# Kernel tuning notes

Measured on AMD Instinct MI355X. Metric: run time of the kernel, lower is better.

## Reference

```python
import jax, jax.numpy as jnp
import numpy as np

NUM_CLASSES = 4
NUM_PROTOTYPE = 8
D = 512
N = 200704  # 16 * 112 * 112 flattened tokens
GAMMA = 0.999        # EMA momentum (self.gamma)
EPS_SINK = 0.05      # sinkhorn epsilon
SINK_ITERS = 3       # sinkhorn iterations


def l2_normalize(x, axis=-1, eps=1e-12):
    n = jnp.linalg.norm(x, axis=axis, keepdims=True)
    return x / jnp.maximum(n, eps)


def layer_norm(x, g, b, eps=1e-5):
    mu = jnp.mean(x, axis=-1, keepdims=True)
    var = jnp.var(x, axis=-1, keepdims=True)
    return (x - mu) / jnp.sqrt(var + eps) * g + b


def masked_sinkhorn(scores, sel):
    # scores: [N, M] similarity to this class's prototypes; sel: [N] bool row mask
    # Faithful masked re-expression of distributed_sinkhorn (which gathers rows
    # where gt_seg == k); zeroed rows contribute nothing to any normalization.
    M = scores.shape[1]
    self32 = sel.astype(scores.dtype)[:, None]
    L = jnp.exp(scores / EPS_SINK) * self32           # [N, M]
    B = jnp.maximum(sel.sum(), 1).astype(scores.dtype)  # number of selected rows
    L = L / jnp.maximum(L.sum(), 1e-30)

    def body(L, _):
        col = L.sum(axis=0, keepdims=True)            # per-prototype mass
        L = L / jnp.maximum(col, 1e-30) / M
        row = L.sum(axis=1, keepdims=True)            # per-token mass
        L = (L / jnp.maximum(row, 1e-30) / B) * self32
        return L, None

    L, _ = jax.lax.scan(body, L, None, length=SINK_ITERS)
    L = L * B
    idx = jnp.argmax(L, axis=1)
    # hard one-hot assignment (deterministic stand-in for hard gumbel_softmax)
    q = jax.nn.one_hot(idx, M, dtype=scores.dtype) * self32
    return q


def prototype_learning(_c, pred, gt_seg, masks, protos, momentum):
    # _c [N, D], pred/gt_seg [N], masks [N, M, K], protos [K, M, D]
    correct = gt_seg == pred
    new_rows = []
    for k in range(NUM_CLASSES):  # small fixed class loop, as in the original
        sel = gt_seg == k
        q = masked_sinkhorn(masks[:, :, k], sel)      # [N, M]
        m_k = (correct & sel).astype(_c.dtype)        # [N]
        m_q = q * m_k[:, None]                        # masked assignments
        c_q = _c * m_k[:, None]                       # masked features
        f = m_q.T @ c_q                               # [M, D] aggregation
        n = m_q.sum(axis=0)                           # [M] per-prototype counts
        f = l2_normalize(f)
        upd = momentum * protos[k] + (1.0 - momentum) * f
        valid = (n != 0) & (sel.sum() > 0) & (n.sum() > 0)
        new_rows.append(jnp.where(valid[:, None], upd, protos[k]))
    return l2_normalize(jnp.stack(new_rows, axis=0))


def reference(feats, ln_gamma, ln_beta, mask_gamma, mask_beta, prototypes, gt_seg):
    _c = l2_normalize(layer_norm(feats, ln_gamma, ln_beta))       # [N, D]
    protos = l2_normalize(prototypes)                             # [K, M, D]
    masks = jnp.einsum('nd,kmd->nmk', _c, protos)                 # [N, M, K]
    out_seg = layer_norm(jnp.max(masks, axis=1), mask_gamma, mask_beta)  # [N, K]
    pred = jnp.argmax(out_seg, axis=1)
    new_protos = prototype_learning(_c, pred, gt_seg.astype(jnp.int32), masks, protos, GAMMA)
    return out_seg, new_protos


def setup_inputs() -> dict:
    key = jax.random.key(0)
    k1, k2, k3 = jax.random.split(key, 3)
    return {
        'feats': jax.random.normal(k1, (N, D), dtype=jnp.float32),
        'ln_gamma': jnp.ones((D,), jnp.float32),
        'ln_beta': jnp.zeros((D,), jnp.float32),
        'mask_gamma': jnp.ones((NUM_CLASSES,), jnp.float32),
        'mask_beta': jnp.zeros((NUM_CLASSES,), jnp.float32),
        'prototypes': 0.02 * jax.random.normal(k2, (NUM_CLASSES, NUM_PROTOTYPE, D), dtype=jnp.float32),
        'gt_seg': jax.random.randint(k3, (N,), 0, NUM_CLASSES, dtype=jnp.int32),
    }
```

## Files before the change

### kernel.cpp

```cpp
#include <hip/hip_runtime.h>
#include <hip/hip_bf16.h>
#include <math.h>

#define NROWS 200704
#define DIM 512
#define NKM 32

#define OFF_RED0   0
#define OFF_RED1   32
#define OFF_RED2   64
#define OFF_CNT    96
#define OFF_NP     100
#define OFF_CUR    192
#define OFF_BASE   2240
#define OFF_FACC   2304
#define ZERO_FLOATS 18688
#define OFF_SUMGP  18688
#define OFF_BP     18720
#define OFF_SCAL   18752
#define OFF_G2GB   18816
#define OFF_PROTON 19840
#define OFF_WHI    36224
#define OFF_WLO    44544
#define OFF_RSTATS 52864
#define OFF_E      855680
#define OFF_FLAGS  2461312
#define OFF_SORT   2662016

typedef __attribute__((ext_vector_type(8)))  short short8;
typedef __attribute__((ext_vector_type(16))) float f32x16;

union ABFrag { unsigned int u[4]; short8 s; };

__device__ __forceinline__ unsigned int pk2(float a, float b) {
    __hip_bfloat162 h2 = __float22bfloat162_rn(make_float2(a, b));
    union { __hip_bfloat162 h; unsigned int u; } cv;
    cv.h = h2;
    return cv.u;
}

__device__ __forceinline__ float block_reduce_sum(float v, float* sm) {
    int t = threadIdx.x;
    sm[t] = v; __syncthreads();
    #pragma unroll
    for (int o = 128; o > 0; o >>= 1) {
        if (t < o) sm[t] += sm[t + o];
        __syncthreads();
    }
    float r = sm[0]; __syncthreads();
    return r;
}

__global__ __launch_bounds__(256) void k_prep(const float* __restrict__ protos,
                                              const float* __restrict__ g,
                                              const float* __restrict__ b,
                                              float* __restrict__ ws) {
    __shared__ float sm[256];
    int t = threadIdx.x, j = blockIdx.x;
    if (j < NKM) {
        const float* p = protos + j * DIM;
        float v = p[t] * p[t] + p[t + 256] * p[t + 256];
        float ss = block_reduce_sum(v, sm);
        float den = fmaxf(sqrtf(ss), 1e-12f);
        float sgp = 0.f, sbp = 0.f;
        unsigned short* whi = (unsigned short*)ws + 2 * OFF_WHI + j * 520;
        unsigned short* wlo = (unsigned short*)ws + 2 * OFF_WLO + j * 520;
        for (int d = t; d < DIM; d += 256) {
            float pn = p[d] / den;
            ws[OFF_PROTON + j * DIM + d] = pn;
            float w = g[d] * pn;
            unsigned int hb = pk2(w, 0.f) & 0xffffu;
            float hf = __uint_as_float(hb << 16);
            unsigned int lb = pk2(w - hf, 0.f) & 0xffffu;
            whi[d] = (unsigned short)hb;
            wlo[d] = (unsigned short)lb;
            sgp += w; sbp += b[d] * pn;
        }
        float s1 = block_reduce_sum(sgp, sm);
        float s2 = block_reduce_sum(sbp, sm);
        if (t == 0) { ws[OFF_SUMGP + j] = s1; ws[OFF_BP + j] = s2; }
    } else {
        float a = 0.f, c = 0.f, e = 0.f;
        for (int d = t; d < DIM; d += 256) {
            float gv = g[d], bv = b[d];
            ws[OFF_G2GB + 2 * d]     = gv * gv;
            ws[OFF_G2GB + 2 * d + 1] = gv * bv;
            a += gv * gv; c += gv * bv; e += bv * bv;
        }
        float s1 = block_reduce_sum(a, sm);
        float s2 = block_reduce_sum(c, sm);
        float s3 = block_reduce_sum(e, sm);
        if (t == 0) { ws[OFF_SCAL] = s1; ws[OFF_SCAL + 1] = s2; ws[OFF_SCAL + 2] = s3; }
    }
}

#define ST1(XV, G2V, GBV) { float _x = (XV); float _x2 = _x * _x; \
    sx += _x; sxx += _x2; \
    sxg2  = fmaf(_x,  (G2V), sxg2); \
    sx2g2 = fmaf(_x2, (G2V), sx2g2); \
    sxgb  = fmaf(_x,  (GBV), sxgb); }

#define PAIRSPLIT(A0, B0, HO, LO) { \
    unsigned int _h = pk2((A0), (B0)); HO = _h; \
    float _ha = __uint_as_float(_h << 16); \
    float _hb = __uint_as_float(_h & 0xffff0000u); \
    LO = pk2((A0) - _ha, (B0) - _hb); }

__global__ __launch_bounds__(256, 2) void k_main(const float* __restrict__ feats,
                                                 const float* __restrict__ mg,
                                                 const float* __restrict__ mb,
                                                 const int* __restrict__ gt_seg,
                                                 float* __restrict__ ws,
                                                 float* __restrict__ out) {
    __shared__ __align__(16) unsigned short ls_whi[32 * 520];
    __shared__ __align__(16) unsigned short ls_wlo[32 * 520];
    __shared__ __align__(16) float ls_g2gb[1024];
    int t = threadIdx.x;
    {
        const float4* sh = (const float4*)(ws + OFF_WHI);
        float4* dh = (float4*)ls_whi;
        for (int i = t; i < 2080; i += 256) dh[i] = sh[i];
        const float4* sl = (const float4*)(ws + OFF_WLO);
        float4* dl = (float4*)ls_wlo;
        for (int i = t; i < 2080; i += 256) dl[i] = sl[i];
        const float4* sg = (const float4*)(ws + OFF_G2GB);
        float4* dg = (float4*)ls_g2gb;
        dg[t] = sg[t];
    }
    __syncthreads();

    int wv = t >> 6, l = t & 63;
    int h = l >> 5, c32 = l & 31;
    int row0 = blockIdx.x * 128 + wv * 32;
    const float* xrow = feats + (size_t)(row0 + c32) * DIM + h * 8;
    const unsigned short* bhp = ls_whi + c32 * 520 + h * 8;
    const unsigned short* blp = ls_wlo + c32 * 520 + h * 8;
    const float4* g4 = ((const float4*)ls_g2gb) + h * 4;

    f32x16 acc;
    #pragma unroll
    for (int i = 0; i < 16; ++i) acc[i] = 0.f;
    float sx = 0.f, sxx = 0.f, sxg2 = 0.f, sx2g2 = 0.f, sxgb = 0.f;

    #pragma unroll 4
    for (int kc = 0; kc < 32; ++kc) {
        float4 xa = *(const float4*)(xrow + kc * 16);
        float4 xb = *(const float4*)(xrow + kc * 16 + 4);
        float4 ga  = g4[kc * 8 + 0];
        float4 gb_ = g4[kc * 8 + 1];
        float4 gc  = g4[kc * 8 + 2];
        float4 gd  = g4[kc * 8 + 3];
        ST1(xa.x, ga.x,  ga.y)  ST1(xa.y, ga.z,  ga.w)
        ST1(xa.z, gb_.x, gb_.y) ST1(xa.w, gb_.z, gb_.w)
        ST1(xb.x, gc.x,  gc.y)  ST1(xb.y, gc.z,  gc.w)
        ST1(xb.z, gd.x,  gd.y)  ST1(xb.w, gd.z,  gd.w)
        ABFrag ah, al;
        PAIRSPLIT(xa.x, xa.y, ah.u[0], al.u[0])
        PAIRSPLIT(xa.z, xa.w, ah.u[1], al.u[1])
        PAIRSPLIT(xb.x, xb.y, ah.u[2], al.u[2])
        PAIRSPLIT(xb.z, xb.w, ah.u[3], al.u[3])
        short8 bh = *(const short8*)(bhp + kc * 16);
        short8 bl = *(const short8*)(blp + kc * 16);
        acc = __builtin_amdgcn_mfma_f32_32x32x16_bf16(ah.s, bh, acc, 0, 0, 0);
        acc = __builtin_amdgcn_mfma_f32_32x32x16_bf16(ah.s, bl, acc, 0, 0, 0);
        acc = __builtin_amdgcn_mfma_f32_32x32x16_bf16(al.s, bh, acc, 0, 0, 0);
    }

    sx    += __shfl_xor(sx, 32, 64);
    sxx   += __shfl_xor(sxx, 32, 64);
    sxg2  += __shfl_xor(sxg2, 32, 64);
    sx2g2 += __shfl_xor(sx2g2, 32, 64);
    sxgb  += __shfl_xor(sxgb, 32, 64);

    float scal0 = ws[OFF_SCAL], scal1 = ws[OFF_SCAL + 1], scal2 = ws[OFF_SCAL + 2];
    float mu  = sx * (1.0f / DIM);
    float var = sxx * (1.0f / DIM) - mu * mu;
    float istd = 1.0f / sqrtf(var + 1e-5f);
    float l2v = istd * istd * (sx2g2 - 2.0f * mu * sxg2 + mu * mu * scal0)
              + 2.0f * istd * (sxgb - mu * scal1) + scal2;
    float L = sqrtf(fmaxf(l2v, 0.0f));
    float invL = 1.0f / fmaxf(L, 1e-12f);
    float aa = istd * invL;
    if (l < 32)
        *(float4*)(ws + OFF_RSTATS + (size_t)(row0 + l) * 4) = make_float4(mu, istd, invL, 0.f);

    float wsum = ws[OFF_SUMGP + c32], wbp = ws[OFF_BP + c32];
    float mg0 = mg[0], mg1 = mg[1], mg2 = mg[2], mg3 = mg[3];
    float mb0 = mb[0], mb1 = mb[1], mb2 = mb[2], mb3 = mb[3];
    int q = c32 >> 3;
    int li8 = c32 & 7;

    #pragma unroll
    for (int r = 0; r < 16; ++r) {
        int rowt = (r & 3) + 8 * (r >> 2) + 4 * h;
        int grow = row0 + rowt;
        float mu_r = __shfl(mu, rowt, 64);
        float aa_r = __shfl(aa, rowt, 64);
        float il_r = __shfl(invL, rowt, 64);
        float s = aa_r * (acc[r] - mu_r * wsum) + il_r * wbp;
        float m = s;
        m = fmaxf(m, __shfl_xor(m, 1, 64));
        m = fmaxf(m, __shfl_xor(m, 2, 64));
        m = fmaxf(m, __shfl_xor(m, 4, 64));
        float vA = m;
        float vB = __shfl_xor(vA, 8, 64);
        float vC = __shfl_xor(vA, 16, 64);
        float vD = __shfl_xor(vB, 16, 64);
        float o0 = (q == 0) ? vA : (q == 1) ? vB : (q == 2) ? vC : vD;
        float o1 = (q == 1) ? vA : (q == 0) ? vB : (q == 3) ? vC : vD;
        float o2 = (q == 2) ? vA : (q == 3) ? vB : (q == 0) ? vC : vD;
        float o3 = (q == 3) ? vA : (q == 2) ? vB : (q == 1) ? vC : vD;
        float mu4 = 0.25f * (o0 + o1 + o2 + o3);
        float e0 = o0 - mu4, e1 = o1 - mu4, e2 = o2 - mu4, e3 = o3 - mu4;
        float v4 = 0.25f * (e0 * e0 + e1 * e1 + e2 * e2 + e3 * e3);
        float is4 = 1.0f / sqrtf(v4 + 1e-5f);
        float f0 = e0 * is4 * mg0 + mb0;
        float f1 = e1 * is4 * mg1 + mb1;
        float f2 = e2 * is4 * mg2 + mb2;
        float f3 = e3 * is4 * mg3 + mb3;
        int pred = 0; float bo = f0;
        if (f1 > bo) { bo = f1; pred = 1; }
        if (f2 > bo) { bo = f2; pred = 2; }
        if (f3 > bo) { bo = f3; pred = 3; }
        int gtv = gt_seg[grow] & 3;
        if (c32 == 0) {
            *(float4*)(out + (size_t)grow * 4) = make_float4(f0, f1, f2, f3);
            ((int*)ws)[OFF_FLAGS + grow] = gtv | ((pred == gtv) ? 4 : 0);
        }
        if (q == gtv) {
            float ev = expf(s * 20.0f);
            ws[OFF_E + (size_t)grow * 8 + li8] = ev;
        }
    }
}

__global__ __launch_bounds__(256) void k_red0(const int* __restrict__ gt_seg,
                                              float* __restrict__ ws) {
    __shared__ float lred[NKM];
    __shared__ int lcnt[4];
    int t = threadIdx.x;
    if (t < NKM) lred[t] = 0.f;
    if (t < 4) lcnt[t] = 0;
    __syncthreads();
    int row = blockIdx.x * 256 + t;
    int gt = gt_seg[row] & 3;
    float4 ea = *(const float4*)(ws + OFF_E + (size_t)row * 8);
    float4 eb = *(const float4*)(ws + OFF_E + (size_t)row * 8 + 4);
    atomicAdd(&lred[gt * 8 + 0], ea.x); atomicAdd(&lred[gt * 8 + 1], ea.y);
    atomicAdd(&lred[gt * 8 + 2], ea.z); atomicAdd(&lred[gt * 8 + 3], ea.w);
    atomicAdd(&lred[gt * 8 + 4], eb.x); atomicAdd(&lred[gt * 8 + 5], eb.y);
    atomicAdd(&lred[gt * 8 + 6], eb.z); atomicAdd(&lred[gt * 8 + 7], eb.w);
    atomicAdd(&lcnt[gt], 1);
    __syncthreads();
    if (t < NKM) atomicAdd(&ws[OFF_RED0 + t], lred[t]);
    if (t < 4) atomicAdd(&((int*)ws)[OFF_CNT + t], lcnt[t]);
}

__global__ __launch_bounds__(256) void k_red1(const int* __restrict__ gt_seg,
                                              float* __restrict__ ws) {
    __shared__ float S0p[4], Bk[4], a1[NKM], lred[NKM];
    int t = threadIdx.x;
    if (t < 4) {
        float s = 0.f;
        #pragma unroll
        for (int m = 0; m < 8; ++m) s += ws[OFF_RED0 + t * 8 + m];
        S0p[t] = fmaxf(s, 1e-30f);
        Bk[t] = fmaxf((float)((const int*)ws)[OFF_CNT + t], 1.0f);
    }
    if (t < NKM) lred[t] = 0.f;
    __syncthreads();
    if (t < NKM) {
        float col = ws[OFF_RED0 + t] / S0p[t >> 3];
        a1[t] = 1.0f / (fmaxf(col, 1e-30f) * 8.0f);
    }
    __syncthreads();
    int row = blockIdx.x * 256 + t;
    int gt = gt_seg[row] & 3;
    float4 ea = *(const float4*)(ws + OFF_E + (size_t)row * 8);
    float4 eb = *(const float4*)(ws + OFF_E + (size_t)row * 8 + 4);
    float ev[8] = {ea.x, ea.y, ea.z, ea.w, eb.x, eb.y, eb.z, eb.w};
    float dotv = 0.f;
    #pragma unroll
    for (int m = 0; m < 8; ++m) dotv += ev[m] * a1[gt * 8 + m];
    float row1 = dotv / S0p[gt];
    float r1 = 1.0f / (fmaxf(row1, 1e-30f) * Bk[gt]);
    #pragma unroll
    for (int m = 0; m < 8; ++m) atomicAdd(&lred[gt * 8 + m], ev[m] * r1);
    __syncthreads();
    if (t < NKM) atomicAdd(&ws[OFF_RED1 + t], lred[t]);
}

__global__ __launch_bounds__(256) void k_red2(const int* __restrict__ gt_seg,
                                              float* __restrict__ ws) {
    __shared__ float S0p[4], Bk[4], a1[NKM], a2[NKM], lred[NKM];
    int t = threadIdx.x;
    if (t < 4) {
        float s = 0.f;
        #pragma unroll
        for (int m = 0; m < 8; ++m) s += ws[OFF_RED0 + t * 8 + m];
        S0p[t] = fmaxf(s, 1e-30f);
        Bk[t] = fmaxf((float)((const int*)ws)[OFF_CNT + t], 1.0f);
    }
    if (t < NKM) lred[t] = 0.f;
    __syncthreads();
    if (t < NKM) {
        float col = ws[OFF_RED0 + t] / S0p[t >> 3];
        a1[t] = 1.0f / (fmaxf(col, 1e-30f) * 8.0f);
    }
    __syncthreads();
    if (t < NKM) {
        float col2 = a1[t] * ws[OFF_RED1 + t] / S0p[t >> 3];
        a2[t] = 1.0f / (fmaxf(col2, 1e-30f) * 8.0f);
    }
    __syncthreads();
    int row = blockIdx.x * 256 + t;
    int gt = gt_seg[row] & 3;
    float4 ea = *(const float4*)(ws + OFF_E + (size_t)row * 8);
    float4 eb = *(const float4*)(ws + OFF_E + (size_t)row * 8 + 4);
    float ev[8] = {ea.x, ea.y, ea.z, ea.w, eb.x, eb.y, eb.z, eb.w};
    float dotv = 0.f;
    #pragma unroll
    for (int m = 0; m < 8; ++m) dotv += ev[m] * a1[gt * 8 + m];
    float row1 = dotv / S0p[gt];
    float r1 = 1.0f / (fmaxf(row1, 1e-30f) * Bk[gt]);
    float dot2 = 0.f;
    #pragma unroll
    for (int m = 0; m < 8; ++m) dot2 += ev[m] * a1[gt * 8 + m] * a2[gt * 8 + m];
    float row2 = dot2 / S0p[gt] * r1;
    float r2 = 1.0f / (fmaxf(row2, 1e-30f) * Bk[gt]);
    #pragma unroll
    for (int m = 0; m < 8; ++m) atomicAdd(&lred[gt * 8 + m], ev[m] * r1 * r2);
    __syncthreads();
    if (t < NKM) atomicAdd(&ws[OFF_RED2 + t], lred[t]);
}

__global__ __launch_bounds__(256) void k_assign(float* __restrict__ ws) {
    __shared__ float S0p[4], Bk[4], a1[NKM], a2[NKM], F[NKM];
    __shared__ int ln[NKM];
    int t = threadIdx.x;
    if (t < 4) {
        float s = 0.f;
        #pragma unroll
        for (int m = 0; m < 8; ++m) s += ws[OFF_RED0 + t * 8 + m];
        S0p[t] = fmaxf(s, 1e-30f);
        Bk[t] = fmaxf((float)((const int*)ws)[OFF_CNT + t], 1.0f);
    }
    if (t < NKM) ln[t] = 0;
    __syncthreads();
    if (t < NKM) {
        float col = ws[OFF_RED0 + t] / S0p[t >> 3];
        a1[t] = 1.0f / (fmaxf(col, 1e-30f) * 8.0f);
    }
    __syncthreads();
    if (t < NKM) {
        float col2 = a1[t] * ws[OFF_RED1 + t] / S0p[t >> 3];
        a2[t] = 1.0f / (fmaxf(col2, 1e-30f) * 8.0f);
    }
    __syncthreads();
    if (t < NKM) {
        float col3 = a1[t] * a2[t] * ws[OFF_RED2 + t] / S0p[t >> 3];
        float a3 = 1.0f / (fmaxf(col3, 1e-30f) * 8.0f);
        F[t] = a1[t] * a2[t] * a3;
    }
    __syncthreads();
    int row = blockIdx.x * 256 + t;
    int flag = ((const int*)ws)[OFF_FLAGS + row];
    int slotv = -1;
    if (flag & 4) {
        int gt = flag & 3;
        float4 ea = *(const float4*)(ws + OFF_E + (size_t)row * 8);
        float4 eb = *(const float4*)(ws + OFF_E + (size_t)row * 8 + 4);
        float ev[8] = {ea.x, ea.y, ea.z, ea.w, eb.x, eb.y, eb.z, eb.w};
        int js = 0; float bv = ev[0] * F[gt * 8];
        #pragma unroll
        for (int m = 1; m < 8; ++m) {
            float v = ev[m] * F[gt * 8 + m];
            if (v > bv) { bv = v; js = m; }
        }
        slotv = gt * 8 + js;
        atomicAdd(&ln[slotv], 1);
    }
    ((int*)ws)[OFF_FLAGS + row] = slotv;
    __syncthreads();
    if (t < NKM && ln[t]) atomicAdd(&((int*)ws)[OFF_NP + t], ln[t]);
}

__global__ void k_prefix(float* __restrict__ ws) {
    if (threadIdx.x == 0) {
        int acc = 0;
        for (int s = 0; s < NKM; ++s) {
            ((int*)ws)[OFF_BASE + s] = acc;
            acc += ((const int*)ws)[OFF_NP + s];
        }
    }
}

__global__ __launch_bounds__(256) void k_scatter(float* __restrict__ ws) {
    int row = blockIdx.x * 256 + threadIdx.x;
    int s = ((const int*)ws)[OFF_FLAGS + row];
    if (s >= 0) {
        int pos = atomicAdd(&((int*)ws)[OFF_CUR + s * 64], 1);
        ((int*)ws)[OFF_SORT + ((const int*)ws)[OFF_BASE + s] + pos] = row;
    }
}

__global__ __launch_bounds__(256) void k_agg(const float* __restrict__ feats,
                                             const float* __restrict__ g,
                                             const float* __restrict__ b,
                                             float* __restrict__ ws) {
    int t = threadIdx.x;
    int slot = blockIdx.x >> 4, ch = blockIdx.x & 15;
    int n = ((const int*)ws)[OFF_NP + slot];
    int base = ((const int*)ws)[OFF_BASE + slot];
    int r0 = base + (ch * n) / 16;
    int r1 = base + ((ch + 1) * n) / 16;
    if (r0 >= r1) return;
    const int* sortl = (const int*)ws + OFF_SORT;
    float2 gv = *(const float2*)(g + 2 * t);
    float2 bv = *(const float2*)(b + 2 * t);
    float acc0 = 0.f, acc1 = 0.f;
    #pragma unroll 4
    for (int i = r0; i < r1; ++i) {
        int row = sortl[i];
        float4 rs = *(const float4*)(ws + OFF_RSTATS + (size_t)row * 4);
        float2 x = *(const float2*)(feats + (size_t)row * DIM + 2 * t);
        acc0 += ((x.x - rs.x) * rs.y * gv.x + bv.x) * rs.z;
        acc1 += ((x.y - rs.x) * rs.y * gv.y + bv.y) * rs.z;
    }
    atomicAdd(&ws[OFF_FACC + slot * DIM + 2 * t],     acc0);
    atomicAdd(&ws[OFF_FACC + slot * DIM + 2 * t + 1], acc1);
}

__global__ __launch_bounds__(256) void k_final(float* __restrict__ ws,
                                               float* __restrict__ out) {
    __shared__ float sm[256];
    int t = threadIdx.x, j = blockIdx.x, k = j >> 3;
    int nj = ((const int*)ws)[OFF_NP + j];
    int ck = ((const int*)ws)[OFF_CNT + k];
    int nsum = 0;
    #pragma unroll
    for (int m = 0; m < 8; ++m) nsum += ((const int*)ws)[OFF_NP + k * 8 + m];
    int d0 = t, d1 = t + 256;
    float f0 = ws[OFF_FACC + j * DIM + d0];
    float f1 = ws[OFF_FACC + j * DIM + d1];
    float nf = block_reduce_sum(f0 * f0 + f1 * f1, sm);
    float fin = 1.0f / fmaxf(sqrtf(nf), 1e-12f);
    float pn0 = ws[OFF_PROTON + j * DIM + d0];
    float pn1 = ws[OFF_PROTON + j * DIM + d1];
    bool valid = (nj != 0) && (ck > 0) && (nsum > 0);
    float r0 = valid ? (0.999f * pn0 + 0.001f * (f0 * fin)) : pn0;
    float r1 = valid ? (0.999f * pn1 + 0.001f * (f1 * fin)) : pn1;
    float n2 = block_reduce_sum(r0 * r0 + r1 * r1, sm);
    float i2 = 1.0f / fmaxf(sqrtf(n2), 1e-12f);
    out[(size_t)NROWS * 4 + j * DIM + d0] = r0 * i2;
    out[(size_t)NROWS * 4 + j * DIM + d1] = r1 * i2;
}

extern "C" void kernel_launch(void* const* d_in, const int* in_sizes, int n_in,
                              void* d_out, int out_size, void* d_ws, size_t ws_size,
                              hipStream_t stream) {
    const float* feats = (const float*)d_in[0];
    const float* ln_g  = (const float*)d_in[1];
    const float* ln_b  = (const float*)d_in[2];
    const float* mg    = (const float*)d_in[3];
    const float* mb    = (const float*)d_in[4];
    const float* prot  = (const float*)d_in[5];
    const int*   gt    = (const int*)d_in[6];
    float* out = (float*)d_out;
    float* ws  = (float*)d_ws;

    hipMemsetAsync(d_ws, 0, ZERO_FLOATS * 4, stream);
    k_prep<<<33, 256, 0, stream>>>(prot, ln_g, ln_b, ws);
    k_main<<<NROWS / 128, 256, 0, stream>>>(feats, mg, mb, gt, ws, out);
    k_red0<<<NROWS / 256, 256, 0, stream>>>(gt, ws);
    k_red1<<<NROWS / 256, 256, 0, stream>>>(gt, ws);
    k_red2<<<NROWS / 256, 256, 0, stream>>>(gt, ws);
    k_assign<<<NROWS / 256, 256, 0, stream>>>(ws);
    k_prefix<<<1, 64, 0, stream>>>(ws);
    k_scatter<<<NROWS / 256, 256, 0, stream>>>(ws);
    k_agg<<<NKM * 16, 256, 0, stream>>>(feats, ln_g, ln_b, ws);
    k_final<<<NKM, 256, 0, stream>>>(ws, out);
}
```

Before: 699.2 us.

## Fuse first sinkhorn reduction into main kernel and drop prefix kernel

The per-class exp-sum and count reduction (k_red0) is folded into k_main using shared-memory atomics, and k_main moves to 1024-thread blocks covering 512 rows so each block loads the bf16 weight tiles into LDS once for four times as many rows. The separate k_prefix launch is removed: k_scatter computes slot bases in shared memory and k_agg recomputes its own base. This saves two kernel launches and one pass over the E buffer. In exchange the larger blocks may lower occupancy or raise register pressure, which the unroll change from 4 to 2 tries to offset, and the launch_bounds of (1024, 4) may be hard for the compiler to meet.

```diff
diff --git a/kernel.cpp b/kernel.cpp
--- a/kernel.cpp
+++ b/kernel.cpp
@@ -106,32 +106,34 @@
     float _hb = __uint_as_float(_h & 0xffff0000u); \
     LO = pk2((A0) - _ha, (B0) - _hb); }
 
-__global__ __launch_bounds__(256, 2) void k_main(const float* __restrict__ feats,
-                                                 const float* __restrict__ mg,
-                                                 const float* __restrict__ mb,
-                                                 const int* __restrict__ gt_seg,
-                                                 float* __restrict__ ws,
-                                                 float* __restrict__ out) {
+__global__ __launch_bounds__(1024, 4) void k_main(const float* __restrict__ feats,
+                                                  const float* __restrict__ mg,
+                                                  const float* __restrict__ mb,
+                                                  const int* __restrict__ gt_seg,
+                                                  float* __restrict__ ws,
+                                                  float* __restrict__ out) {
     __shared__ __align__(16) unsigned short ls_whi[32 * 520];
     __shared__ __align__(16) unsigned short ls_wlo[32 * 520];
     __shared__ __align__(16) float ls_g2gb[1024];
+    __shared__ float s_lred[NKM];
+    __shared__ int s_lcnt[4];
     int t = threadIdx.x;
     {
         const float4* sh = (const float4*)(ws + OFF_WHI);
         float4* dh = (float4*)ls_whi;
-        for (int i = t; i < 2080; i += 256) dh[i] = sh[i];
+        for (int i = t; i < 2080; i += 1024) dh[i] = sh[i];
         const float4* sl = (const float4*)(ws + OFF_WLO);
         float4* dl = (float4*)ls_wlo;
-        for (int i = t; i < 2080; i += 256) dl[i] = sl[i];
-        const float4* sg = (const float4*)(ws + OFF_G2GB);
-        float4* dg = (float4*)ls_g2gb;
-        dg[t] = sg[t];
+        for (int i = t; i < 2080; i += 1024) dl[i] = sl[i];
+        if (t < 256) ((float4*)ls_g2gb)[t] = ((const float4*)(ws + OFF_G2GB))[t];
+        if (t < NKM) s_lred[t] = 0.f;
+        if (t < 4) s_lcnt[t] = 0;
     }
     __syncthreads();
 
     int wv = t >> 6, l = t & 63;
     int h = l >> 5, c32 = l & 31;
-    int row0 = blockIdx.x * 128 + wv * 32;
+    int row0 = blockIdx.x * 512 + wv * 32;
     const float* xrow = feats + (size_t)(row0 + c32) * DIM + h * 8;
     const unsigned short* bhp = ls_whi + c32 * 520 + h * 8;
     const unsigned short* blp = ls_wlo + c32 * 520 + h * 8;
@@ -142,7 +144,7 @@
     for (int i = 0; i < 16; ++i) acc[i] = 0.f;
     float sx = 0.f, sxx = 0.f, sxg2 = 0.f, sx2g2 = 0.f, sxgb = 0.f;
 
-    #pragma unroll 4
+    #pragma unroll 2
     for (int kc = 0; kc < 32; ++kc) {
         float4 xa = *(const float4*)(xrow + kc * 16);
         float4 xb = *(const float4*)(xrow + kc * 16 + 4);
@@ -230,30 +232,13 @@
         if (q == gtv) {
             float ev = expf(s * 20.0f);
             ws[OFF_E + (size_t)grow * 8 + li8] = ev;
+            atomicAdd(&s_lred[(q << 3) + li8], ev);
+            if (li8 == 0) atomicAdd(&s_lcnt[q], 1);
         }
     }
-}
-
-__global__ __launch_bounds__(256) void k_red0(const int* __restrict__ gt_seg,
-                                              float* __restrict__ ws) {
-    __shared__ float lred[NKM];
-    __shared__ int lcnt[4];
-    int t = threadIdx.x;
-    if (t < NKM) lred[t] = 0.f;
-    if (t < 4) lcnt[t] = 0;
-    __syncthreads();
-    int row = blockIdx.x * 256 + t;
-    int gt = gt_seg[row] & 3;
-    float4 ea = *(const float4*)(ws + OFF_E + (size_t)row * 8);
-    float4 eb = *(const float4*)(ws + OFF_E + (size_t)row * 8 + 4);
-    atomicAdd(&lred[gt * 8 + 0], ea.x); atomicAdd(&lred[gt * 8 + 1], ea.y);
-    atomicAdd(&lred[gt * 8 + 2], ea.z); atomicAdd(&lred[gt * 8 + 3], ea.w);
-    atomicAdd(&lred[gt * 8 + 4], eb.x); atomicAdd(&lred[gt * 8 + 5], eb.y);
-    atomicAdd(&lred[gt * 8 + 6], eb.z); atomicAdd(&lred[gt * 8 + 7], eb.w);
-    atomicAdd(&lcnt[gt], 1);
-    __syncthreads();
-    if (t < NKM) atomicAdd(&ws[OFF_RED0 + t], lred[t]);
-    if (t < 4) atomicAdd(&((int*)ws)[OFF_CNT + t], lcnt[t]);
+    __syncthreads();
+    if (t < NKM) atomicAdd(&ws[OFF_RED0 + t], s_lred[t]);
+    if (t < 4) atomicAdd(&((int*)ws)[OFF_CNT + t], s_lcnt[t]);
 }
 
 __global__ __launch_bounds__(256) void k_red1(const int* __restrict__ gt_seg,
@@ -385,22 +370,20 @@
     if (t < NKM && ln[t]) atomicAdd(&((int*)ws)[OFF_NP + t], ln[t]);
 }
 
-__global__ void k_prefix(float* __restrict__ ws) {
-    if (threadIdx.x == 0) {
+__global__ __launch_bounds__(256) void k_scatter(float* __restrict__ ws) {
+    __shared__ int s_base[NKM];
+    int t = threadIdx.x;
+    if (t == 0) {
         int acc = 0;
-        for (int s = 0; s < NKM; ++s) {
-            ((int*)ws)[OFF_BASE + s] = acc;
-            acc += ((const int*)ws)[OFF_NP + s];
-        }
-    }
-}
-
-__global__ __launch_bounds__(256) void k_scatter(float* __restrict__ ws) {
-    int row = blockIdx.x * 256 + threadIdx.x;
+        #pragma unroll
+        for (int s = 0; s < NKM; ++s) { s_base[s] = acc; acc += ((const int*)ws)[OFF_NP + s]; }
+    }
+    __syncthreads();
+    int row = blockIdx.x * 256 + t;
     int s = ((const int*)ws)[OFF_FLAGS + row];
     if (s >= 0) {
         int pos = atomicAdd(&((int*)ws)[OFF_CUR + s * 64], 1);
-        ((int*)ws)[OFF_SORT + ((const int*)ws)[OFF_BASE + s] + pos] = row;
+        ((int*)ws)[OFF_SORT + s_base[s] + pos] = row;
     }
 }
 
@@ -408,10 +391,17 @@
                                              const float* __restrict__ g,
                                              const float* __restrict__ b,
                                              float* __restrict__ ws) {
+    __shared__ int s_bn[2];
     int t = threadIdx.x;
     int slot = blockIdx.x >> 4, ch = blockIdx.x & 15;
-    int n = ((const int*)ws)[OFF_NP + slot];
-    int base = ((const int*)ws)[OFF_BASE + slot];
+    if (t == 0) {
+        int acc = 0;
+        for (int s = 0; s < slot; ++s) acc += ((const int*)ws)[OFF_NP + s];
+        s_bn[0] = acc;
+        s_bn[1] = ((const int*)ws)[OFF_NP + slot];
+    }
+    __syncthreads();
+    int base = s_bn[0], n = s_bn[1];
     int r0 = base + (ch * n) / 16;
     int r1 = base + ((ch + 1) * n) / 16;
     if (r0 >= r1) return;
@@ -471,12 +461,10 @@
 
     hipMemsetAsync(d_ws, 0, ZERO_FLOATS * 4, stream);
     k_prep<<<33, 256, 0, stream>>>(prot, ln_g, ln_b, ws);
-    k_main<<<NROWS / 128, 256, 0, stream>>>(feats, mg, mb, gt, ws, out);
-    k_red0<<<NROWS / 256, 256, 0, stream>>>(gt, ws);
+    k_main<<<NROWS / 512, 1024, 0, stream>>>(feats, mg, mb, gt, ws, out);
     k_red1<<<NROWS / 256, 256, 0, stream>>>(gt, ws);
     k_red2<<<NROWS / 256, 256, 0, stream>>>(gt, ws);
     k_assign<<<NROWS / 256, 256, 0, stream>>>(ws);
-    k_prefix<<<1, 64, 0, stream>>>(ws);
     k_scatter<<<NROWS / 256, 256, 0, stream>>>(ws);
     k_agg<<<NKM * 16, 256, 0, stream>>>(feats, ln_g, ln_b, ws);
     k_final<<<NKM, 256, 0, stream>>>(ws, out);
```

Result: faster. 681.7 us (-2.5%).
